# Kernel tuning notes

Hardware: AMD Instinct MI355X
Metric: run time of the kernel (lower is better)

Reference implementation:

```python
import jax, jax.numpy as jnp
import numpy as np

DIST_SCALE = 10000.0   # divisor in kernel()
KERNEL_EPS = 0.0001    # additive epsilon before reciprocal


def setup_inputs() -> dict:
    key = jax.random.key(0)
    k1, k2, k3 = jax.random.split(key, 3)
    batch, keysize, dict_size, categories = 4096, 512, 16384, 128
    x = jax.random.normal(k1, (batch, keysize), dtype=jnp.float32)
    # keras TruncatedNormal(mean=0, stddev=3) approximated by scaled normal
    keys = 3.0 * jax.random.normal(k2, (dict_size, keysize), dtype=jnp.float32)
    V = jax.random.normal(k3, (dict_size, categories), dtype=jnp.float32)
    return {"x": x, "keys": keys, "V": V}


def reference(x, keys, V):
    # sq_distance(keys, x): (dict_size, batch)
    sq = (
        jnp.sum(keys * keys, axis=1, keepdims=True)            # (D, 1)
        - 2.0 * jnp.einsum("dk,bk->db", keys, x)               # (D, B)
        + jnp.sum(x * x, axis=1)[None, :]                      # (1, B)
    )
    kern = 1.0 / (sq / DIST_SCALE + KERNEL_EPS)                # (D, B)
    KV = jnp.einsum("db,dc->bc", kern, V)                      # (B, C)
    # original: diag(1 / (KV @ ones)) @ KV  ==  row-normalize by row sum
    return KV / jnp.sum(KV, axis=1, keepdims=True)
```

## Files before the change

kernel.cpp:

```cpp
#include <hip/hip_runtime.h>

#define BATCH 4096
#define DICT  16384
#define KDIM  512
#define CAT   128
#define ND    16
#define DSLICE (DICT/ND)
#define DCH   64
#define BT    128

typedef __attribute__((ext_vector_type(4))) float          f32x4;
typedef __attribute__((ext_vector_type(8))) short          short8;
typedef __attribute__((ext_vector_type(8))) unsigned short ushort8;

__device__ __forceinline__ unsigned short f2bf(float f) {
  unsigned int u = __float_as_uint(f);
  return (unsigned short)((u + 0x7fffu + ((u >> 16) & 1u)) >> 16);
}

#define AS1 __attribute__((address_space(1)))
#define AS3 __attribute__((address_space(3)))
__device__ __forceinline__ void gl_lds16(const void* g, void* l) {
  __builtin_amdgcn_global_load_lds((AS1 void*)(g), (AS3 void*)(l), 16, 0, 0);
}

__global__ void prep_rows(const float* __restrict__ in,
                          unsigned short* __restrict__ ob,
                          float* __restrict__ sums) {
  const int lane = threadIdx.x & 63, wv = threadIdx.x >> 6;
  const int row = blockIdx.x * 4 + wv;
  const float* rp = in + ((size_t)row << 9);
  float4 a = *(const float4*)(rp + lane * 8);
  float4 b = *(const float4*)(rp + lane * 8 + 4);
  float s = a.x*a.x + a.y*a.y + a.z*a.z + a.w*a.w
          + b.x*b.x + b.y*b.y + b.z*b.z + b.w*b.w;
  ushort8 o;
  o[0]=f2bf(a.x); o[1]=f2bf(a.y); o[2]=f2bf(a.z); o[3]=f2bf(a.w);
  o[4]=f2bf(b.x); o[5]=f2bf(b.y); o[6]=f2bf(b.z); o[7]=f2bf(b.w);
  *(ushort8*)(ob + ((size_t)row << 9) + lane * 8) = o;
  #pragma unroll
  for (int m = 32; m; m >>= 1) s += __shfl_xor(s, m);
  if (lane == 0) sums[row] = s;
}

__global__ void prep_vt(const float* __restrict__ V,
                        unsigned short* __restrict__ Vt) {
  __shared__ float t[64][129];
  const int d0 = blockIdx.x * 64;
  const int tid = threadIdx.x;
  #pragma unroll
  for (int j = 0; j < 32; ++j) {
    int idx = j * 256 + tid;
    t[idx >> 7][idx & 127] = V[((size_t)d0 << 7) + idx];
  }
  __syncthreads();
  #pragma unroll
  for (int j = 0; j < 32; ++j) {
    int idx = j * 256 + tid;
    int cc = idx >> 6, dd = idx & 63;
    Vt[((size_t)cc << 14) + d0 + dd] = f2bf(t[dd][cc]);
  }
}

__global__ __launch_bounds__(256, 2)
void varkeys_fused(const unsigned short* __restrict__ xb,
                   const unsigned short* __restrict__ kb,
                   const unsigned short* __restrict__ vt,
                   const float* __restrict__ sx,
                   const float* __restrict__ sk,
                   float* __restrict__ kvp) {
  __shared__ __attribute__((aligned(16))) char lds[61440];
  char* As = lds;
  char* Bs = lds + 8192;
  char* Vs = lds + 24576;
  char* Ps = lds + 40960;
  float* sks = (float*)(lds + 57344);

  const int tid  = threadIdx.x;
  const int lane = tid & 63;
  const int wv   = tid >> 6;
  const int c    = lane & 15;
  const int h    = lane >> 4;
  const int sw   = (lane & 7) << 4;

  const int bid    = blockIdx.x;
  const int btile  = bid & 31;
  const int dslice = bid >> 5;
  const int b0     = btile * BT;
  const int dbase  = dslice * DSLICE;

  { f32x4 v = *(const f32x4*)(sk + dbase + tid * 4);
    *(f32x4*)(sks + tid * 4) = v; }
  const float sxv0 = sx[b0 + wv * 32 + c];
  const float sxv1 = sx[b0 + wv * 32 + 16 + c];

  const f32x4 zero = {0.f, 0.f, 0.f, 0.f};
  f32x4 acc[2][8];
  #pragma unroll
  for (int i = 0; i < 2; ++i)
    #pragma unroll
    for (int j = 0; j < 8; ++j) acc[i][j] = zero;

  const char* xbB = (const char*)xb;
  const char* kbB = (const char*)kb;
  const char* vtB = (const char*)vt;

  for (int dc = 0; dc < DSLICE / DCH; ++dc) {
    const int dg = dbase + dc * DCH;

    f32x4 S[4][2];
    #pragma unroll
    for (int i = 0; i < 4; ++i) { S[i][0] = zero; S[i][1] = zero; }

    for (int kk = 0; kk < KDIM / 64; ++kk) {
      __syncthreads();
      #pragma unroll
      for (int r = 0; r < 2; ++r) {
        int L = r * 4096 + wv * 1024 + lane * 16;
        int row = L >> 7, inb = L & 127;
        gl_lds16(kbB + (((size_t)(dg + row)) << 10) + (kk << 7) + (inb ^ ((row & 7) << 4)),
                 As + r * 4096 + wv * 1024);
      }
      #pragma unroll
      for (int r = 0; r < 4; ++r) {
        int L = r * 4096 + wv * 1024 + lane * 16;
        int row = L >> 7, inb = L & 127;
        gl_lds16(xbB + (((size_t)(b0 + row)) << 10) + (kk << 7) + (inb ^ ((row & 7) << 4)),
                 Bs + r * 4096 + wv * 1024);
      }
      if (kk == 0) {
        #pragma unroll
        for (int r = 0; r < 4; ++r) {
          int L = r * 4096 + wv * 1024 + lane * 16;
          int row = L >> 7, inb = L & 127;
          gl_lds16(vtB + (((size_t)row) << 15) + ((size_t)dg << 1) + (inb ^ ((row & 7) << 4)),
                   Vs + r * 4096 + wv * 1024);
        }
      }
      __syncthreads();

      #pragma unroll
      for (int kf = 0; kf < 2; ++kf) {
        const int ko = (kf * 64 + h * 16) ^ sw;
        short8 bf0 = *(const short8*)(Bs + ((wv * 32 + c) << 7) + ko);
        short8 bf1 = *(const short8*)(Bs + ((wv * 32 + 16 + c) << 7) + ko);
        #pragma unroll
        for (int i = 0; i < 4; ++i) {
          short8 af = *(const short8*)(As + ((i * 16 + c) << 7) + ko);
          S[i][0] = __builtin_amdgcn_mfma_f32_16x16x32_bf16(af, bf0, S[i][0], 0, 0, 0);
          S[i][1] = __builtin_amdgcn_mfma_f32_16x16x32_bf16(af, bf1, S[i][1], 0, 0, 0);
        }
      }
    }

    #pragma unroll
    for (int i = 0; i < 4; ++i) {
      const f32x4 skv = *(const f32x4*)(sks + dc * 64 + i * 16 + h * 4);
      #pragma unroll
      for (int fj = 0; fj < 2; ++fj) {
        const float sxv = fj ? sxv1 : sxv0;
        f32x4 s = S[i][fj];
        float k0 = 10000.f * __builtin_amdgcn_rcpf(skv[0] + sxv - 2.f * s[0] + 1.f);
        float k1 = 10000.f * __builtin_amdgcn_rcpf(skv[1] + sxv - 2.f * s[1] + 1.f);
        float k2 = 10000.f * __builtin_amdgcn_rcpf(skv[2] + sxv - 2.f * s[2] + 1.f);
        float k3 = 10000.f * __builtin_amdgcn_rcpf(skv[3] + sxv - 2.f * s[3] + 1.f);
        unsigned int w0 = (unsigned int)f2bf(k0) | ((unsigned int)f2bf(k1) << 16);
        unsigned int w1 = (unsigned int)f2bf(k2) | ((unsigned int)f2bf(k3) << 16);
        int b = fj * 16 + c;
        char* p = Ps + (wv << 12) + (b << 7) + ((i * 32 + h * 8) ^ sw);
        ((unsigned int*)p)[0] = w0;
        ((unsigned int*)p)[1] = w1;
      }
    }

    #pragma unroll
    for (int dk = 0; dk < 2; ++dk) {
      const int ko = (dk * 64 + h * 16) ^ sw;
      short8 pa0 = *(const short8*)(Ps + (wv << 12) + (c << 7) + ko);
      short8 pa1 = *(const short8*)(Ps + (wv << 12) + ((16 + c) << 7) + ko);
      #pragma unroll
      for (int fc = 0; fc < 8; ++fc) {
        short8 vb = *(const short8*)(Vs + ((fc * 16 + c) << 7) + ko);
        acc[0][fc] = __builtin_amdgcn_mfma_f32_16x16x32_bf16(pa0, vb, acc[0][fc], 0, 0, 0);
        acc[1][fc] = __builtin_amdgcn_mfma_f32_16x16x32_bf16(pa1, vb, acc[1][fc], 0, 0, 0);
      }
    }
  }

  float* op = kvp + (((size_t)dslice * BATCH + b0 + wv * 32) << 7);
  #pragma unroll
  for (int fb = 0; fb < 2; ++fb)
    #pragma unroll
    for (int r = 0; r < 4; ++r) {
      int brow = fb * 16 + h * 4 + r;
      #pragma unroll
      for (int fc = 0; fc < 8; ++fc)
        op[((size_t)brow << 7) + fc * 16 + c] = acc[fb][fc][r];
    }
}

__global__ void reduce_norm(const float* __restrict__ part, float* __restrict__ out) {
  const int lane = threadIdx.x & 63, wv = threadIdx.x >> 6;
  const int b = blockIdx.x * 4 + wv;
  float v0 = 0.f, v1 = 0.f;
  #pragma unroll
  for (int s = 0; s < ND; ++s) {
    const float* p = part + ((((size_t)s << 12) + b) << 7);
    v0 += p[lane]; v1 += p[lane + 64];
  }
  float t = v0 + v1;
  #pragma unroll
  for (int m = 32; m; m >>= 1) t += __shfl_xor(t, m);
  out[((size_t)b << 7) + lane]      = v0 / t;
  out[((size_t)b << 7) + lane + 64] = v1 / t;
}

extern "C" void kernel_launch(void* const* d_in, const int* in_sizes, int n_in,
                              void* d_out, int out_size, void* d_ws, size_t ws_size,
                              hipStream_t stream) {
  (void)in_sizes; (void)n_in; (void)out_size; (void)ws_size;
  const float* x    = (const float*)d_in[0];
  const float* keys = (const float*)d_in[1];
  const float* V    = (const float*)d_in[2];
  float* out = (float*)d_out;
  char* ws = (char*)d_ws;
  unsigned short* xb = (unsigned short*)(ws);
  unsigned short* kb = (unsigned short*)(ws + ((size_t)4 << 20));
  unsigned short* vt = (unsigned short*)(ws + ((size_t)20 << 20));
  float* sx  = (float*)(ws + ((size_t)24 << 20));
  float* sk  = (float*)(ws + ((size_t)24 << 20) + (1 << 16));
  float* kvp = (float*)(ws + ((size_t)25 << 20));

  prep_rows<<<BATCH / 4, 256, 0, stream>>>(x, xb, sx);
  prep_rows<<<DICT / 4, 256, 0, stream>>>(keys, kb, sk);
  prep_vt<<<DICT / 64, 256, 0, stream>>>(V, vt);
  varkeys_fused<<<(BATCH / BT) * ND, 256, 0, stream>>>(xb, kb, vt, sx, sk, kvp);
  reduce_norm<<<BATCH / 4, 256, 0, stream>>>(kvp, out);
}
```

Measured before the change: 143.9 us.

## Switch fused kernel to 32x32x16 MFMA with 128-wide dict chunks and adaptive split

Rewrites the fused distance/kernel/aggregation kernel to use 32x32x16 bf16 MFMA tiles with a 2x2 wave layout, 128-row dictionary chunks, and new XOR swizzles for LDS. The P buffer now reuses the A/B staging area, which cuts LDS use and allows 3 blocks per CU. V-tile loads are spread across the last k-iterations and a second half load. The dictionary split count goes to 32 when the workspace is large enough. The aim is fewer LDS reads per flop and more parallelism, at the cost of extra barriers and larger partial buffers to reduce.

New measurement: 229.2 us. 59.3% more time.

```diff
diff --git a/kernel.cpp b/kernel.cpp
--- a/kernel.cpp
+++ b/kernel.cpp
@@ -4,14 +4,14 @@
 #define DICT  16384
 #define KDIM  512
 #define CAT   128
-#define ND    16
-#define DSLICE (DICT/ND)
-#define DCH   64
 #define BT    128
-
-typedef __attribute__((ext_vector_type(4))) float          f32x4;
-typedef __attribute__((ext_vector_type(8))) short          short8;
-typedef __attribute__((ext_vector_type(8))) unsigned short ushort8;
+#define DCH   128
+
+typedef __attribute__((ext_vector_type(4)))  float f32x4;
+typedef __attribute__((ext_vector_type(16))) float f32x16;
+typedef __attribute__((ext_vector_type(8)))  short short8;
+typedef __attribute__((ext_vector_type(8)))  unsigned short ushort8;
+typedef __attribute__((ext_vector_type(2)))  unsigned int uintx2;
 
 __device__ __forceinline__ unsigned short f2bf(float f) {
   unsigned int u = __float_as_uint(f);
@@ -23,6 +23,8 @@
 __device__ __forceinline__ void gl_lds16(const void* g, void* l) {
   __builtin_amdgcn_global_load_lds((AS1 void*)(g), (AS3 void*)(l), 16, 0, 0);
 }
+
+#define MFMA32(a, b, c) __builtin_amdgcn_mfma_f32_32x32x16_bf16((a), (b), (c), 0, 0, 0)
 
 __global__ void prep_rows(const float* __restrict__ in,
                           unsigned short* __restrict__ ob,
@@ -62,149 +64,172 @@
   }
 }
 
-__global__ __launch_bounds__(256, 2)
+__global__ __launch_bounds__(256, 3)
 void varkeys_fused(const unsigned short* __restrict__ xb,
                    const unsigned short* __restrict__ kb,
                    const unsigned short* __restrict__ vt,
                    const float* __restrict__ sx,
                    const float* __restrict__ sk,
-                   float* __restrict__ kvp) {
-  __shared__ __attribute__((aligned(16))) char lds[61440];
-  char* As = lds;
-  char* Bs = lds + 8192;
-  char* Vs = lds + 24576;
-  char* Ps = lds + 40960;
-  float* sks = (float*)(lds + 57344);
-
-  const int tid  = threadIdx.x;
-  const int lane = tid & 63;
-  const int wv   = tid >> 6;
-  const int c    = lane & 15;
-  const int h    = lane >> 4;
-  const int sw   = (lane & 7) << 4;
-
-  const int bid    = blockIdx.x;
-  const int btile  = bid & 31;
-  const int dslice = bid >> 5;
-  const int b0     = btile * BT;
-  const int dbase  = dslice * DSLICE;
-
-  { f32x4 v = *(const f32x4*)(sk + dbase + tid * 4);
-    *(f32x4*)(sks + tid * 4) = v; }
-  const float sxv0 = sx[b0 + wv * 32 + c];
-  const float sxv1 = sx[b0 + wv * 32 + 16 + c];
-
-  const f32x4 zero = {0.f, 0.f, 0.f, 0.f};
-  f32x4 acc[2][8];
-  #pragma unroll
-  for (int i = 0; i < 2; ++i)
-    #pragma unroll
-    for (int j = 0; j < 8; ++j) acc[i][j] = zero;
+                   float* __restrict__ kvp,
+                   int dsl, int ndc) {
+  __shared__ __attribute__((aligned(16))) char lds[53248];
+  char* const As = lds;
+  char* const Bs = lds + 16384;
+  char* const Vs = lds + 32768;
+  char* const Ps = lds;
+  float* const sks = (float*)(lds + 49152);
+
+  const int tid = threadIdx.x;
+  const int lane = tid & 63, h = lane >> 5, r31 = lane & 31;
+  const int wv = tid >> 6;
+  const int dw = wv >> 1, bw = wv & 1;
+  const int bw2 = wv >> 1, cw2 = wv & 1;
+
+  const int bid = blockIdx.x;
+  const int btile = bid & 31, dslice = bid >> 5;
+  const int b0 = btile * BT;
+  const int dbase = dslice * dsl;
+
+  if (tid * 4 < dsl) {
+    f32x4 v = *(const f32x4*)(sk + dbase + tid * 4);
+    *(f32x4*)(sks + tid * 4) = v;
+  }
+  const float sxv0 = sx[b0 + bw * 64 + r31];
+  const float sxv1 = sx[b0 + bw * 64 + 32 + r31];
+
+  const int sex   = (tid & 15) ^ (tid >> 4);
+  const int srow  = 2 * (tid >> 4) + (sex >> 3);
+  const int skoff = (sex & 7) << 4;
+  const size_t ksrc_t = (size_t)srow * 1024 + skoff;
+  const size_t vsrc_t = (size_t)srow * 32768 + skoff;
+
+  const int MH  = (((r31 & 1) << 3) | h) ^ (r31 >> 1);
+  int T[4];
+  #pragma unroll
+  for (int ks = 0; ks < 4; ++ks) T[ks] = ((ks << 1) ^ MH) << 4;
+  const int PSW = (r31 & 15) << 4;
+  const int PH  = (h << 4) ^ PSW;
+  const int PW  = (h << 3) ^ PSW;
+  const int arb = (dw * 32 + (r31 >> 1)) * 256;
+  const int brb = (bw * 32 + (r31 >> 1)) * 256;
+  const int vrb = (cw2 * 32 + (r31 >> 1)) * 256;
+  const int prb = (bw2 * 64 + r31) * 256;
+  const int pwb = (bw * 64 + r31) * 256;
 
   const char* xbB = (const char*)xb;
   const char* kbB = (const char*)kb;
   const char* vtB = (const char*)vt;
 
-  for (int dc = 0; dc < DSLICE / DCH; ++dc) {
-    const int dg = dbase + dc * DCH;
-
-    f32x4 S[4][2];
-    #pragma unroll
-    for (int i = 0; i < 4; ++i) { S[i][0] = zero; S[i][1] = zero; }
+  const f32x16 z16 = {0.f};
+  f32x16 acc[2][2];
+  acc[0][0] = z16; acc[0][1] = z16; acc[1][0] = z16; acc[1][1] = z16;
+
+  for (int dc = 0; dc < ndc; ++dc) {
+    const int dg0 = dbase + dc * DCH;
+    f32x16 S00 = z16, S01 = z16, S10 = z16, S11 = z16;
 
     for (int kk = 0; kk < KDIM / 64; ++kk) {
       __syncthreads();
-      #pragma unroll
-      for (int r = 0; r < 2; ++r) {
-        int L = r * 4096 + wv * 1024 + lane * 16;
-        int row = L >> 7, inb = L & 127;
-        gl_lds16(kbB + (((size_t)(dg + row)) << 10) + (kk << 7) + (inb ^ ((row & 7) << 4)),
-                 As + r * 4096 + wv * 1024);
-      }
-      #pragma unroll
-      for (int r = 0; r < 4; ++r) {
-        int L = r * 4096 + wv * 1024 + lane * 16;
-        int row = L >> 7, inb = L & 127;
-        gl_lds16(xbB + (((size_t)(b0 + row)) << 10) + (kk << 7) + (inb ^ ((row & 7) << 4)),
-                 Bs + r * 4096 + wv * 1024);
-      }
-      if (kk == 0) {
+      const size_t ksrc = (size_t)dg0 * 1024 + (size_t)(kk * 128) + ksrc_t;
+      const size_t xsrc = (size_t)b0 * 1024 + (size_t)(kk * 128) + ksrc_t;
+      #pragma unroll
+      for (int p = 0; p < 4; ++p) {
+        gl_lds16(kbB + ksrc + (size_t)p * 32768, As + p * 4096 + wv * 1024);
+        gl_lds16(xbB + xsrc + (size_t)p * 32768, Bs + p * 4096 + wv * 1024);
+      }
+      if (kk >= 6) {
+        const size_t vsrc = vsrc_t + (size_t)dg0 * 2;
         #pragma unroll
-        for (int r = 0; r < 4; ++r) {
-          int L = r * 4096 + wv * 1024 + lane * 16;
-          int row = L >> 7, inb = L & 127;
-          gl_lds16(vtB + (((size_t)row) << 15) + ((size_t)dg << 1) + (inb ^ ((row & 7) << 4)),
-                   Vs + r * 4096 + wv * 1024);
+        for (int pp = 0; pp < 2; ++pp) {
+          int p = (kk - 6) * 2 + pp;
+          gl_lds16(vtB + vsrc + (size_t)p * 1048576, Vs + p * 4096 + wv * 1024);
         }
       }
       __syncthreads();
-
-      #pragma unroll
-      for (int kf = 0; kf < 2; ++kf) {
-        const int ko = (kf * 64 + h * 16) ^ sw;
-        short8 bf0 = *(const short8*)(Bs + ((wv * 32 + c) << 7) + ko);
-        short8 bf1 = *(const short8*)(Bs + ((wv * 32 + 16 + c) << 7) + ko);
+      #pragma unroll
+      for (int ks = 0; ks < 4; ++ks) {
+        short8 a0 = *(const short8*)(As + arb + T[ks]);
+        short8 a1 = *(const short8*)(As + arb + 4096 + T[ks]);
+        short8 bf0 = *(const short8*)(Bs + brb + T[ks]);
+        short8 bf1 = *(const short8*)(Bs + brb + 4096 + T[ks]);
+        S00 = MFMA32(a0, bf0, S00);
+        S01 = MFMA32(a0, bf1, S01);
+        S10 = MFMA32(a1, bf0, S10);
+        S11 = MFMA32(a1, bf1, S11);
+      }
+    }
+
+    __syncthreads();
+
+    const float* sksb = sks + dc * DCH + dw * 64 + h * 4;
+    #pragma unroll
+    for (int i = 0; i < 2; ++i) {
+      #pragma unroll
+      for (int j = 0; j < 2; ++j) {
+        const float sxv = j ? sxv1 : sxv0;
+        const f32x16 s = (i == 0) ? (j == 0 ? S00 : S01) : (j == 0 ? S10 : S11);
+        char* pw = Ps + pwb + j * 8192;
         #pragma unroll
-        for (int i = 0; i < 4; ++i) {
-          short8 af = *(const short8*)(As + ((i * 16 + c) << 7) + ko);
-          S[i][0] = __builtin_amdgcn_mfma_f32_16x16x32_bf16(af, bf0, S[i][0], 0, 0, 0);
-          S[i][1] = __builtin_amdgcn_mfma_f32_16x16x32_bf16(af, bf1, S[i][1], 0, 0, 0);
+        for (int q = 0; q < 4; ++q) {
+          f32x4 skv = *(const f32x4*)(sksb + i * 32 + q * 8);
+          float k0 = 10000.f * __builtin_amdgcn_rcpf(skv[0] + sxv - 2.f * s[q*4+0] + 1.f);
+          float k1 = 10000.f * __builtin_amdgcn_rcpf(skv[1] + sxv - 2.f * s[q*4+1] + 1.f);
+          float k2 = 10000.f * __builtin_amdgcn_rcpf(skv[2] + sxv - 2.f * s[q*4+2] + 1.f);
+          float k3 = 10000.f * __builtin_amdgcn_rcpf(skv[3] + sxv - 2.f * s[q*4+3] + 1.f);
+          uintx2 w;
+          w[0] = (unsigned int)f2bf(k0) | ((unsigned int)f2bf(k1) << 16);
+          w[1] = (unsigned int)f2bf(k2) | ((unsigned int)f2bf(k3) << 16);
+          *(uintx2*)(pw + ((dw * 128 + i * 64 + q * 16) ^ PW)) = w;
         }
       }
     }
+    __syncthreads();
 
     #pragma unroll
-    for (int i = 0; i < 4; ++i) {
-      const f32x4 skv = *(const f32x4*)(sks + dc * 64 + i * 16 + h * 4);
-      #pragma unroll
-      for (int fj = 0; fj < 2; ++fj) {
-        const float sxv = fj ? sxv1 : sxv0;
-        f32x4 s = S[i][fj];
-        float k0 = 10000.f * __builtin_amdgcn_rcpf(skv[0] + sxv - 2.f * s[0] + 1.f);
-        float k1 = 10000.f * __builtin_amdgcn_rcpf(skv[1] + sxv - 2.f * s[1] + 1.f);
-        float k2 = 10000.f * __builtin_amdgcn_rcpf(skv[2] + sxv - 2.f * s[2] + 1.f);
-        float k3 = 10000.f * __builtin_amdgcn_rcpf(skv[3] + sxv - 2.f * s[3] + 1.f);
-        unsigned int w0 = (unsigned int)f2bf(k0) | ((unsigned int)f2bf(k1) << 16);
-        unsigned int w1 = (unsigned int)f2bf(k2) | ((unsigned int)f2bf(k3) << 16);
-        int b = fj * 16 + c;
-        char* p = Ps + (wv << 12) + (b << 7) + ((i * 32 + h * 8) ^ sw);
-        ((unsigned int*)p)[0] = w0;
-        ((unsigned int*)p)[1] = w1;
+    for (int half = 0; half < 2; ++half) {
+      if (half) {
+        __syncthreads();
+        const size_t vsrc = vsrc_t + (size_t)(dg0 + 64) * 2;
+        #pragma unroll
+        for (int p = 0; p < 4; ++p)
+          gl_lds16(vtB + vsrc + (size_t)p * 1048576, Vs + p * 4096 + wv * 1024);
+        __syncthreads();
+      }
+      #pragma unroll
+      for (int dk2 = 0; dk2 < 4; ++dk2) {
+        const int du = ((half * 4 + dk2) << 5) ^ PH;
+        short8 pa0 = *(const short8*)(Ps + prb + du);
+        short8 pa1 = *(const short8*)(Ps + prb + 8192 + du);
+        short8 v0 = *(const short8*)(Vs + vrb + T[dk2]);
+        short8 v1 = *(const short8*)(Vs + vrb + 4096 + T[dk2]);
+        acc[0][0] = MFMA32(pa0, v0, acc[0][0]);
+        acc[0][1] = MFMA32(pa0, v1, acc[0][1]);
+        acc[1][0] = MFMA32(pa1, v0, acc[1][0]);
+        acc[1][1] = MFMA32(pa1, v1, acc[1][1]);
       }
     }
-
+  }
+
+  float* outb = kvp + ((size_t)(dslice * BATCH + b0 + bw2 * 64) << 7) + cw2 * 64;
+  #pragma unroll
+  for (int jm = 0; jm < 2; ++jm)
     #pragma unroll
-    for (int dk = 0; dk < 2; ++dk) {
-      const int ko = (dk * 64 + h * 16) ^ sw;
-      short8 pa0 = *(const short8*)(Ps + (wv << 12) + (c << 7) + ko);
-      short8 pa1 = *(const short8*)(Ps + (wv << 12) + ((16 + c) << 7) + ko);
-      #pragma unroll
-      for (int fc = 0; fc < 8; ++fc) {
-        short8 vb = *(const short8*)(Vs + ((fc * 16 + c) << 7) + ko);
-        acc[0][fc] = __builtin_amdgcn_mfma_f32_16x16x32_bf16(pa0, vb, acc[0][fc], 0, 0, 0);
-        acc[1][fc] = __builtin_amdgcn_mfma_f32_16x16x32_bf16(pa1, vb, acc[1][fc], 0, 0, 0);
-      }
-    }
-  }
-
-  float* op = kvp + (((size_t)dslice * BATCH + b0 + wv * 32) << 7);
-  #pragma unroll
-  for (int fb = 0; fb < 2; ++fb)
-    #pragma unroll
-    for (int r = 0; r < 4; ++r) {
-      int brow = fb * 16 + h * 4 + r;
-      #pragma unroll
-      for (int fc = 0; fc < 8; ++fc)
-        op[((size_t)brow << 7) + fc * 16 + c] = acc[fb][fc][r];
-    }
-}
-
-__global__ void reduce_norm(const float* __restrict__ part, float* __restrict__ out) {
+    for (int q = 0; q < 4; ++q)
+      #pragma unroll
+      for (int rr = 0; rr < 4; ++rr) {
+        int brow = jm * 32 + q * 8 + h * 4 + rr;
+        float* o = outb + ((size_t)brow << 7);
+        o[r31]      = acc[jm][0][q * 4 + rr];
+        o[32 + r31] = acc[jm][1][q * 4 + rr];
+      }
+}
+
+__global__ void reduce_norm(const float* __restrict__ part, float* __restrict__ out,
+                            int nd) {
   const int lane = threadIdx.x & 63, wv = threadIdx.x >> 6;
   const int b = blockIdx.x * 4 + wv;
   float v0 = 0.f, v1 = 0.f;
-  #pragma unroll
-  for (int s = 0; s < ND; ++s) {
+  for (int s = 0; s < nd; ++s) {
     const float* p = part + ((((size_t)s << 12) + b) << 7);
     v0 += p[lane]; v1 += p[lane + 64];
   }
@@ -218,7 +243,7 @@
 extern "C" void kernel_launch(void* const* d_in, const int* in_sizes, int n_in,
                               void* d_out, int out_size, void* d_ws, size_t ws_size,
                               hipStream_t stream) {
-  (void)in_sizes; (void)n_in; (void)out_size; (void)ws_size;
+  (void)in_sizes; (void)n_in; (void)out_size;
   const float* x    = (const float*)d_in[0];
   const float* keys = (const float*)d_in[1];
   const float* V    = (const float*)d_in[2];
@@ -231,9 +256,13 @@
   float* sk  = (float*)(ws + ((size_t)24 << 20) + (1 << 16));
   float* kvp = (float*)(ws + ((size_t)25 << 20));
 
+  const int nd  = (ws_size >= ((size_t)90 << 20)) ? 32 : 16;
+  const int dsl = DICT / nd;
+  const int ndc = dsl / DCH;
+
   prep_rows<<<BATCH / 4, 256, 0, stream>>>(x, xb, sx);
   prep_rows<<<DICT / 4, 256, 0, stream>>>(keys, kb, sk);
   prep_vt<<<DICT / 64, 256, 0, stream>>>(V, vt);
-  varkeys_fused<<<(BATCH / BT) * ND, 256, 0, stream>>>(xb, kb, vt, sx, sk, kvp);
-  reduce_norm<<<BATCH / 4, 256, 0, stream>>>(kvp, out);
-}
+  varkeys_fused<<<32 * nd, 256, 0, stream>>>(xb, kb, vt, sx, sk, kvp, dsl, ndc);
+  reduce_norm<<<BATCH / 4, 256, 0, stream>>>(kvp, out, nd);
+}
```

## Double-buffer key/x LDS tiles and read V fragments directly from global

Applied to the files above, without the earlier changes.

The key and x bf16 tiles are now staged into two LDS buffers. The next k-step's async global-to-LDS loads are issued before computing on the current buffer, and one of the two barriers per k-step is dropped. This is meant to hide global load latency behind the distance MFMAs. V fragments for the second GEMM are read straight from global memory instead of being staged in LDS once per chunk. LDS use grows to about 68KB per block, and correctness relies on the async LDS loads having completed by the single remaining barrier.

Result: slower. 167.4 us (+16.4%).

```diff
diff --git a/kernel.cpp b/kernel.cpp
--- a/kernel.cpp
+++ b/kernel.cpp
@@ -23,6 +23,8 @@
 __device__ __forceinline__ void gl_lds16(const void* g, void* l) {
   __builtin_amdgcn_global_load_lds((AS1 void*)(g), (AS3 void*)(l), 16, 0, 0);
 }
+
+#define MFMA16(a, b, c) __builtin_amdgcn_mfma_f32_16x16x32_bf16((a), (b), (c), 0, 0, 0)
 
 __global__ void prep_rows(const float* __restrict__ in,
                           unsigned short* __restrict__ ob,
@@ -69,12 +71,9 @@
                    const float* __restrict__ sx,
                    const float* __restrict__ sk,
                    float* __restrict__ kvp) {
-  __shared__ __attribute__((aligned(16))) char lds[61440];
-  char* As = lds;
-  char* Bs = lds + 8192;
-  char* Vs = lds + 24576;
-  char* Ps = lds + 40960;
-  float* sks = (float*)(lds + 57344);
+  __shared__ __attribute__((aligned(16))) char lds[69632];
+  char* const Ps = lds + 49152;
+  float* const sks = (float*)(lds + 65536);
 
   const int tid  = threadIdx.x;
   const int lane = tid & 63;
@@ -94,17 +93,42 @@
   const float sxv0 = sx[b0 + wv * 32 + c];
   const float sxv1 = sx[b0 + wv * 32 + 16 + c];
 
-  const f32x4 zero = {0.f, 0.f, 0.f, 0.f};
-  f32x4 acc[2][8];
-  #pragma unroll
-  for (int i = 0; i < 2; ++i)
-    #pragma unroll
-    for (int j = 0; j < 8; ++j) acc[i][j] = zero;
+  int rwA[2], ofA[2], rwB[4], ofB[4];
+  #pragma unroll
+  for (int r = 0; r < 4; ++r) {
+    int L = r * 4096 + wv * 1024 + lane * 16;
+    int row = L >> 7, inb = L & 127;
+    if (r < 2) { rwA[r] = row; ofA[r] = inb ^ ((row & 7) << 4); }
+    rwB[r] = row; ofB[r] = inb ^ ((row & 7) << 4);
+  }
 
   const char* xbB = (const char*)xb;
   const char* kbB = (const char*)kb;
   const char* vtB = (const char*)vt;
 
+  const f32x4 zero = {0.f, 0.f, 0.f, 0.f};
+  f32x4 acc[2][8];
+  #pragma unroll
+  for (int i = 0; i < 2; ++i)
+    #pragma unroll
+    for (int j = 0; j < 8; ++j) acc[i][j] = zero;
+
+  auto stage = [&](int dg2, int kbyte, int buf) {
+    char* A2 = lds + buf * 8192;
+    char* B2 = lds + 16384 + buf * 16384;
+    #pragma unroll
+    for (int r = 0; r < 2; ++r)
+      gl_lds16(kbB + (((size_t)(dg2 + rwA[r])) << 10) + kbyte + ofA[r],
+               A2 + r * 4096 + wv * 1024);
+    #pragma unroll
+    for (int r = 0; r < 4; ++r)
+      gl_lds16(xbB + (((size_t)(b0 + rwB[r])) << 10) + kbyte + ofB[r],
+               B2 + r * 4096 + wv * 1024);
+  };
+
+  int cur = 0;
+  stage(dbase, 0, 0);
+
   for (int dc = 0; dc < DSLICE / DCH; ++dc) {
     const int dg = dbase + dc * DCH;
 
@@ -112,33 +136,15 @@
     #pragma unroll
     for (int i = 0; i < 4; ++i) { S[i][0] = zero; S[i][1] = zero; }
 
+    #pragma unroll
     for (int kk = 0; kk < KDIM / 64; ++kk) {
       __syncthreads();
-      #pragma unroll
-      for (int r = 0; r < 2; ++r) {
-        int L = r * 4096 + wv * 1024 + lane * 16;
-        int row = L >> 7, inb = L & 127;
-        gl_lds16(kbB + (((size_t)(dg + row)) << 10) + (kk << 7) + (inb ^ ((row & 7) << 4)),
-                 As + r * 4096 + wv * 1024);
-      }
-      #pragma unroll
-      for (int r = 0; r < 4; ++r) {
-        int L = r * 4096 + wv * 1024 + lane * 16;
-        int row = L >> 7, inb = L & 127;
-        gl_lds16(xbB + (((size_t)(b0 + row)) << 10) + (kk << 7) + (inb ^ ((row & 7) << 4)),
-                 Bs + r * 4096 + wv * 1024);
-      }
-      if (kk == 0) {
-        #pragma unroll
-        for (int r = 0; r < 4; ++r) {
-          int L = r * 4096 + wv * 1024 + lane * 16;
-          int row = L >> 7, inb = L & 127;
-          gl_lds16(vtB + (((size_t)row) << 15) + ((size_t)dg << 1) + (inb ^ ((row & 7) << 4)),
-                   Vs + r * 4096 + wv * 1024);
-        }
-      }
-      __syncthreads();
-
+      const int ns = dc * 8 + kk + 1;
+      if (ns < 128)
+        stage(dbase + (ns >> 3) * DCH, (ns & 7) << 7, cur ^ 1);
+
+      const char* As = lds + cur * 8192;
+      const char* Bs = lds + 16384 + cur * 16384;
       #pragma unroll
       for (int kf = 0; kf < 2; ++kf) {
         const int ko = (kf * 64 + h * 16) ^ sw;
@@ -147,10 +153,11 @@
         #pragma unroll
         for (int i = 0; i < 4; ++i) {
           short8 af = *(const short8*)(As + ((i * 16 + c) << 7) + ko);
-          S[i][0] = __builtin_amdgcn_mfma_f32_16x16x32_bf16(af, bf0, S[i][0], 0, 0, 0);
-          S[i][1] = __builtin_amdgcn_mfma_f32_16x16x32_bf16(af, bf1, S[i][1], 0, 0, 0);
+          S[i][0] = MFMA16(af, bf0, S[i][0]);
+          S[i][1] = MFMA16(af, bf1, S[i][1]);
         }
       }
+      cur ^= 1;
     }
 
     #pragma unroll
@@ -178,11 +185,13 @@
       const int ko = (dk * 64 + h * 16) ^ sw;
       short8 pa0 = *(const short8*)(Ps + (wv << 12) + (c << 7) + ko);
       short8 pa1 = *(const short8*)(Ps + (wv << 12) + ((16 + c) << 7) + ko);
+      const char* vbase = vtB + ((size_t)c << 15)
+                        + ((size_t)(dg + dk * 32 + h * 8) << 1);
       #pragma unroll
       for (int fc = 0; fc < 8; ++fc) {
-        short8 vb = *(const short8*)(Vs + ((fc * 16 + c) << 7) + ko);
-        acc[0][fc] = __builtin_amdgcn_mfma_f32_16x16x32_bf16(pa0, vb, acc[0][fc], 0, 0, 0);
-        acc[1][fc] = __builtin_amdgcn_mfma_f32_16x16x32_bf16(pa1, vb, acc[1][fc], 0, 0, 0);
+        short8 vb = *(const short8*)(vbase + ((size_t)fc << 19));
+        acc[0][fc] = MFMA16(pa0, vb, acc[0][fc]);
+        acc[1][fc] = MFMA16(pa1, vb, acc[1][fc]);
       }
     }
   }
@@ -234,6 +243,6 @@
   prep_rows<<<BATCH / 4, 256, 0, stream>>>(x, xb, sx);
   prep_rows<<<DICT / 4, 256, 0, stream>>>(keys, kb, sk);
   prep_vt<<<DICT / 64, 256, 0, stream>>>(V, vt);
-  varkeys_fused<<<(BATCH / BT) * ND, 256, 0, stream>>>(xb, kb, vt, sx, sk, kvp);
+  varkeys_fused<<<32 * ND, 256, 0, stream>>>(xb, kb, vt, sx, sk, kvp);
   reduce_norm<<<BATCH / 4, 256, 0, stream>>>(kvp, out);
 }
```
